# Performance work log

Hardware: AMD Instinct MI355X
Metric: run time of the kernel (lower is better)

Reference implementation:

```python
import jax, jax.numpy as jnp
import numpy as np

NUM_SAMPLE = 10


def setup_inputs() -> dict:
    key = jax.random.key(0)
    k1, k2, k3, k4, k5 = jax.random.split(key, 5)
    N, F, B, S = 100000, 256, 20000, NUM_SAMPLE
    features_ue = jax.random.normal(k1, (N, F), dtype=jnp.float32)
    features_ap = jax.random.normal(k2, (N, F), dtype=jnp.float32)
    neigh_idx = jax.random.randint(k3, (B, S), 0, N, dtype=jnp.int32)
    nodes = jax.random.randint(k4, (B,), 0, N, dtype=jnp.int32)
    # xavier-uniform weight [embed_dim, feature_dim] = [256, 2*F]
    embed_dim, feature_dim = 256, 2 * F
    limit = float(np.sqrt(6.0 / (embed_dim + feature_dim)))
    weight = jax.random.uniform(k5, (embed_dim, feature_dim), dtype=jnp.float32,
                                minval=-limit, maxval=limit)
    return {"features_ue": features_ue, "features_ap": features_ap,
            "neigh_idx": neigh_idx, "nodes": nodes, "weight": weight}


def reference(features_ue, features_ap, neigh_idx, nodes, weight):
    # sample_model='ue2ue': other_feature = self_feature = features_ue
    S = neigh_idx.shape[1]
    # gather sampled neighbor features: [B, S, F] -> sum over S
    gathered = jnp.take(features_ue, neigh_idx, axis=0)
    # original: mask.div(num_neigh + 1), i.e. divide by count PLUS one
    neigh_feats = gathered.sum(axis=1) / jnp.float32(S + 1)  # [B, F]
    self_feats = jnp.take(features_ue, nodes, axis=0)        # [B, F]
    combined = jnp.concatenate([self_feats, neigh_feats], axis=1)  # [B, 2F]
    # weight.mm(combined.t()) then relu -> [embed_dim, B]
    out = jax.nn.relu(jnp.einsum('ef,bf->eb', weight, combined))
    return out
```

## Files before the change

kernel.cpp:

```cpp
#include <hip/hip_runtime.h>

typedef __attribute__((ext_vector_type(8))) short short8;
typedef __attribute__((ext_vector_type(4))) float f32x4;

#define B_TOTAL 20000
#define B_PAD   20096
#define NF      256
#define K2      512
#define NS      10

__device__ __forceinline__ unsigned short f2bf(float x) {
    unsigned u = __builtin_bit_cast(unsigned, x);
    u += 0x7FFFu + ((u >> 16) & 1u);
    return (unsigned short)(u >> 16);
}

__global__ __launch_bounds__(256) void gather_combine(
    const float* __restrict__ ue, const int* __restrict__ nidx,
    const int* __restrict__ nodes, const float* __restrict__ w,
    unsigned short* __restrict__ comb, unsigned short* __restrict__ wbf)
{
    const int t = threadIdx.x, blk = blockIdx.x;
    if (blk < 128) {
        const int base = blk * 1024 + t * 4;
        const float4 v = *(const float4*)(w + base);
        ushort4 o;
        o.x = f2bf(v.x); o.y = f2bf(v.y); o.z = f2bf(v.z); o.w = f2bf(v.w);
        *(ushort4*)(wbf + base) = o;
    }
    const int lane = t & 63;
    const int b = blk * 4 + (t >> 6);
    if (b >= B_PAD) return;
    unsigned short* crow = comb + (size_t)b * K2;
    if (b < B_TOTAL) {
        const int node = nodes[b];
        const float4 sf = ((const float4*)(ue + (size_t)node * NF))[lane];
        int myidx = 0;
        if (lane < NS) myidx = nidx[b * NS + lane];
        float ax = 0.f, ay = 0.f, az = 0.f, aw = 0.f;
        #pragma unroll
        for (int s = 0; s < NS; ++s) {
            const int is = __shfl(myidx, s);
            const float4 v = ((const float4*)(ue + (size_t)is * NF))[lane];
            ax += v.x; ay += v.y; az += v.z; aw += v.w;
        }
        const float inv = 1.0f / 11.0f;
        ushort4 s4, n4;
        s4.x = f2bf(sf.x); s4.y = f2bf(sf.y); s4.z = f2bf(sf.z); s4.w = f2bf(sf.w);
        n4.x = f2bf(ax * inv); n4.y = f2bf(ay * inv); n4.z = f2bf(az * inv); n4.w = f2bf(aw * inv);
        *(ushort4*)(crow + lane * 4) = s4;
        *(ushort4*)(crow + NF + lane * 4) = n4;
    } else {
        ushort4 z; z.x = z.y = z.z = z.w = 0;
        *(ushort4*)(crow + lane * 4) = z;
        *(ushort4*)(crow + NF + lane * 4) = z;
    }
}

__global__ __launch_bounds__(256) void gemm_relu(
    const unsigned short* __restrict__ wbf,
    const unsigned short* __restrict__ comb,
    float* __restrict__ out)
{
    __shared__ unsigned short Alds[4096];
    __shared__ unsigned short Blds[4096];
    const int t    = threadIdx.x;
    const int lane = t & 63;
    const int wv   = t >> 6;
    const int wm   = wv >> 1, wn = wv & 1;
    const int n0   = blockIdx.x * 128;
    const int m0   = blockIdx.y * 128;
    const int srow = t & 127;
    const int skg  = t >> 7;
    const int fr   = lane & 15;
    const int kq   = lane >> 4;

    f32x4 acc[4][4] = {};

    const short8* A8 = (const short8*)Alds;
    const short8* B8 = (const short8*)Blds;

    for (int ks = 0; ks < 16; ++ks) {
        const unsigned short* ga = wbf  + (size_t)(m0 + srow) * K2 + ks * 32 + skg * 8;
        const unsigned short* gb = comb + (size_t)(n0 + srow) * K2 + ks * 32 + skg * 8;
        unsigned short* la = Alds + t * 8;
        unsigned short* lb = Blds + t * 8;
        __builtin_amdgcn_global_load_lds((const __attribute__((address_space(1))) void*)ga,
            (__attribute__((address_space(3))) void*)la, 16, 0, 0);
        __builtin_amdgcn_global_load_lds((const __attribute__((address_space(1))) void*)(ga + 16),
            (__attribute__((address_space(3))) void*)(la + 2048), 16, 0, 0);
        __builtin_amdgcn_global_load_lds((const __attribute__((address_space(1))) void*)gb,
            (__attribute__((address_space(3))) void*)lb, 16, 0, 0);
        __builtin_amdgcn_global_load_lds((const __attribute__((address_space(1))) void*)(gb + 16),
            (__attribute__((address_space(3))) void*)(lb + 2048), 16, 0, 0);
        asm volatile("s_waitcnt vmcnt(0)" ::: "memory");
        __syncthreads();

        short8 af[4], bg[4];
        #pragma unroll
        for (int i = 0; i < 4; ++i)
            af[i] = A8[kq * 128 + wm * 64 + i * 16 + fr];
        #pragma unroll
        for (int j = 0; j < 4; ++j)
            bg[j] = B8[kq * 128 + wn * 64 + j * 16 + fr];
        #pragma unroll
        for (int i = 0; i < 4; ++i)
            #pragma unroll
            for (int j = 0; j < 4; ++j)
                acc[i][j] = __builtin_amdgcn_mfma_f32_16x16x32_bf16(af[i], bg[j], acc[i][j], 0, 0, 0);
        __syncthreads();
    }

    #pragma unroll
    for (int i = 0; i < 4; ++i) {
        const int e = m0 + wm * 64 + i * 16 + kq * 4;
        #pragma unroll
        for (int j = 0; j < 4; ++j) {
            const int b = n0 + wn * 64 + j * 16 + fr;
            if (b < B_TOTAL) {
                #pragma unroll
                for (int r = 0; r < 4; ++r)
                    out[(size_t)(e + r) * B_TOTAL + b] = fmaxf(acc[i][j][r], 0.0f);
            }
        }
    }
}

extern "C" void kernel_launch(void* const* d_in, const int* in_sizes, int n_in,
                              void* d_out, int out_size, void* d_ws, size_t ws_size,
                              hipStream_t stream) {
    const float* ue    = (const float*)d_in[0];
    const int*   nidx  = (const int*)d_in[2];
    const int*   nodes = (const int*)d_in[3];
    const float* w     = (const float*)d_in[4];
    float*       out   = (float*)d_out;

    unsigned short* comb = (unsigned short*)d_ws;
    unsigned short* wbf  = comb + (size_t)B_PAD * K2;

    hipLaunchKernelGGL(gather_combine, dim3(B_PAD / 4), dim3(256), 0, stream,
                       ue, nidx, nodes, w, comb, wbf);
    hipLaunchKernelGGL(gemm_relu, dim3(B_PAD / 128, 2), dim3(256), 0, stream,
                       wbf, comb, out);
}
```

Baseline: 60.64 us.

## Fuse neighbor gather with GEMM, keeping combined tile in swizzled LDS

Weight conversion moves into its own small kernel. The gather/mean and the GEMM are fused: each block gathers 32 batch rows into a swizzled bf16 LDS tile and multiplies it against all 256 weight rows, which are loaded straight from global/L2 into registers. This removes the global round trip of the combined bf16 matrix and the per-k-step syncs. In exchange, each block rereads the whole weight matrix and the tiles are smaller, so the MFMA work per load drops.

```diff
diff --git a/kernel.cpp b/kernel.cpp
--- a/kernel.cpp
+++ b/kernel.cpp
@@ -4,7 +4,8 @@
 typedef __attribute__((ext_vector_type(4))) float f32x4;
 
 #define B_TOTAL 20000
-#define B_PAD   20096
+#define BT      32
+#define NBLK    625
 #define NF      256
 #define K2      512
 #define NS      10
@@ -15,113 +16,97 @@
     return (unsigned short)(u >> 16);
 }
 
-__global__ __launch_bounds__(256) void gather_combine(
-    const float* __restrict__ ue, const int* __restrict__ nidx,
-    const int* __restrict__ nodes, const float* __restrict__ w,
-    unsigned short* __restrict__ comb, unsigned short* __restrict__ wbf)
-{
-    const int t = threadIdx.x, blk = blockIdx.x;
-    if (blk < 128) {
-        const int base = blk * 1024 + t * 4;
-        const float4 v = *(const float4*)(w + base);
-        ushort4 o;
-        o.x = f2bf(v.x); o.y = f2bf(v.y); o.z = f2bf(v.z); o.w = f2bf(v.w);
-        *(ushort4*)(wbf + base) = o;
-    }
-    const int lane = t & 63;
-    const int b = blk * 4 + (t >> 6);
-    if (b >= B_PAD) return;
-    unsigned short* crow = comb + (size_t)b * K2;
-    if (b < B_TOTAL) {
-        const int node = nodes[b];
-        const float4 sf = ((const float4*)(ue + (size_t)node * NF))[lane];
-        int myidx = 0;
-        if (lane < NS) myidx = nidx[b * NS + lane];
-        float ax = 0.f, ay = 0.f, az = 0.f, aw = 0.f;
-        #pragma unroll
-        for (int s = 0; s < NS; ++s) {
-            const int is = __shfl(myidx, s);
-            const float4 v = ((const float4*)(ue + (size_t)is * NF))[lane];
-            ax += v.x; ay += v.y; az += v.z; aw += v.w;
-        }
-        const float inv = 1.0f / 11.0f;
-        ushort4 s4, n4;
-        s4.x = f2bf(sf.x); s4.y = f2bf(sf.y); s4.z = f2bf(sf.z); s4.w = f2bf(sf.w);
-        n4.x = f2bf(ax * inv); n4.y = f2bf(ay * inv); n4.z = f2bf(az * inv); n4.w = f2bf(aw * inv);
-        *(ushort4*)(crow + lane * 4) = s4;
-        *(ushort4*)(crow + NF + lane * 4) = n4;
-    } else {
-        ushort4 z; z.x = z.y = z.z = z.w = 0;
-        *(ushort4*)(crow + lane * 4) = z;
-        *(ushort4*)(crow + NF + lane * 4) = z;
-    }
+__global__ __launch_bounds__(256) void wconvert(const float* __restrict__ w,
+                                                unsigned short* __restrict__ wbf) {
+    const int i = (blockIdx.x * 256 + threadIdx.x) * 4;
+    const float4 v = *(const float4*)(w + i);
+    ushort4 o;
+    o.x = f2bf(v.x); o.y = f2bf(v.y); o.z = f2bf(v.z); o.w = f2bf(v.w);
+    *(ushort4*)(wbf + i) = o;
 }
 
-__global__ __launch_bounds__(256) void gemm_relu(
-    const unsigned short* __restrict__ wbf,
-    const unsigned short* __restrict__ comb,
+__global__ __launch_bounds__(256) void fused(
+    const float* __restrict__ ue, const int* __restrict__ nidx,
+    const int* __restrict__ nodes, const unsigned short* __restrict__ wbf,
     float* __restrict__ out)
 {
-    __shared__ unsigned short Alds[4096];
-    __shared__ unsigned short Blds[4096];
+    __shared__ unsigned short comb[64 * BT * 8];
     const int t    = threadIdx.x;
     const int lane = t & 63;
     const int wv   = t >> 6;
-    const int wm   = wv >> 1, wn = wv & 1;
-    const int n0   = blockIdx.x * 128;
-    const int m0   = blockIdx.y * 128;
-    const int srow = t & 127;
-    const int skg  = t >> 7;
-    const int fr   = lane & 15;
-    const int kq   = lane >> 4;
+    const int n0   = blockIdx.x * BT;
 
-    f32x4 acc[4][4] = {};
+    {
+        const int r0 = wv * 8;
+        const int b0 = n0 + r0;
+        const int idxA = nidx[b0 * NS + lane];
+        const int idxB = (lane < 16) ? nidx[b0 * NS + 64 + lane] : 0;
+        const int nodv = (lane < 8) ? nodes[b0 + lane] : 0;
 
-    const short8* A8 = (const short8*)Alds;
-    const short8* B8 = (const short8*)Blds;
+        const int kcS   = lane >> 1;
+        const int swz   = (kcS & 7) << 4;
+        const int half8 = (lane & 1) * 8;
 
+        #pragma unroll
+        for (int r = 0; r < 8; ++r) {
+            const int row = r0 + r;
+            const int nd  = __shfl(nodv, r);
+            const float4 sf = ((const float4*)(ue + (size_t)nd * NF))[lane];
+            float ax = 0.f, ay = 0.f, az = 0.f, aw = 0.f;
+            #pragma unroll
+            for (int s = 0; s < NS; ++s) {
+                const int p  = r * NS + s;
+                const int is = (p < 64) ? __shfl(idxA, p) : __shfl(idxB, p - 64);
+                const float4 v = ((const float4*)(ue + (size_t)is * NF))[lane];
+                ax += v.x; ay += v.y; az += v.z; aw += v.w;
+            }
+            const float inv = 1.0f / 11.0f;
+            ushort4 s4, n4;
+            s4.x = f2bf(sf.x); s4.y = f2bf(sf.y); s4.z = f2bf(sf.z); s4.w = f2bf(sf.w);
+            n4.x = f2bf(ax * inv); n4.y = f2bf(ay * inv);
+            n4.z = f2bf(az * inv); n4.w = f2bf(aw * inv);
+            const int byteS = (((kcS       ) * BT + row) * 16 + half8) ^ swz;
+            const int byteN = (((kcS + 32  ) * BT + row) * 16 + half8) ^ swz;
+            *(ushort4*)((char*)comb + byteS) = s4;
+            *(ushort4*)((char*)comb + byteN) = n4;
+        }
+    }
+    __syncthreads();
+
+    const int fr = lane & 15;
+    const int kq = lane >> 4;
+    const unsigned short* wp = wbf + (size_t)(wv * 64 + fr) * K2 + kq * 8;
+
+    f32x4 acc[4][2] = {};
+    #pragma unroll
     for (int ks = 0; ks < 16; ++ks) {
-        const unsigned short* ga = wbf  + (size_t)(m0 + srow) * K2 + ks * 32 + skg * 8;
-        const unsigned short* gb = comb + (size_t)(n0 + srow) * K2 + ks * 32 + skg * 8;
-        unsigned short* la = Alds + t * 8;
-        unsigned short* lb = Blds + t * 8;
-        __builtin_amdgcn_global_load_lds((const __attribute__((address_space(1))) void*)ga,
-            (__attribute__((address_space(3))) void*)la, 16, 0, 0);
-        __builtin_amdgcn_global_load_lds((const __attribute__((address_space(1))) void*)(ga + 16),
-            (__attribute__((address_space(3))) void*)(la + 2048), 16, 0, 0);
-        __builtin_amdgcn_global_load_lds((const __attribute__((address_space(1))) void*)gb,
-            (__attribute__((address_space(3))) void*)lb, 16, 0, 0);
-        __builtin_amdgcn_global_load_lds((const __attribute__((address_space(1))) void*)(gb + 16),
-            (__attribute__((address_space(3))) void*)(lb + 2048), 16, 0, 0);
-        asm volatile("s_waitcnt vmcnt(0)" ::: "memory");
-        __syncthreads();
-
-        short8 af[4], bg[4];
+        short8 af[4];
         #pragma unroll
         for (int i = 0; i < 4; ++i)
-            af[i] = A8[kq * 128 + wm * 64 + i * 16 + fr];
+            af[i] = *(const short8*)(wp + (size_t)i * 16 * K2 + ks * 32);
+        short8 bg[2];
+        const int kc = ks * 4 + kq;
         #pragma unroll
-        for (int j = 0; j < 4; ++j)
-            bg[j] = B8[kq * 128 + wn * 64 + j * 16 + fr];
+        for (int j = 0; j < 2; ++j) {
+            const int byte = ((kc * BT + j * 16 + fr) * 16) ^ ((kc & 7) << 4);
+            bg[j] = *(const short8*)((const char*)comb + byte);
+        }
         #pragma unroll
         for (int i = 0; i < 4; ++i)
             #pragma unroll
-            for (int j = 0; j < 4; ++j)
+            for (int j = 0; j < 2; ++j)
                 acc[i][j] = __builtin_amdgcn_mfma_f32_16x16x32_bf16(af[i], bg[j], acc[i][j], 0, 0, 0);
-        __syncthreads();
     }
 
     #pragma unroll
     for (int i = 0; i < 4; ++i) {
-        const int e = m0 + wm * 64 + i * 16 + kq * 4;
+        const int e = wv * 64 + i * 16 + kq * 4;
         #pragma unroll
-        for (int j = 0; j < 4; ++j) {
-            const int b = n0 + wn * 64 + j * 16 + fr;
-            if (b < B_TOTAL) {
-                #pragma unroll
-                for (int r = 0; r < 4; ++r)
-                    out[(size_t)(e + r) * B_TOTAL + b] = fmaxf(acc[i][j][r], 0.0f);
-            }
+        for (int j = 0; j < 2; ++j) {
+            const int b = n0 + j * 16 + fr;
+            #pragma unroll
+            for (int r = 0; r < 4; ++r)
+                out[(size_t)(e + r) * B_TOTAL + b] = fmaxf(acc[i][j][r], 0.0f);
         }
     }
 }
@@ -135,11 +120,9 @@
     const float* w     = (const float*)d_in[4];
     float*       out   = (float*)d_out;
 
-    unsigned short* comb = (unsigned short*)d_ws;
-    unsigned short* wbf  = comb + (size_t)B_PAD * K2;
+    unsigned short* wbf = (unsigned short*)d_ws;
 
-    hipLaunchKernelGGL(gather_combine, dim3(B_PAD / 4), dim3(256), 0, stream,
-                       ue, nidx, nodes, w, comb, wbf);
-    hipLaunchKernelGGL(gemm_relu, dim3(B_PAD / 128, 2), dim3(256), 0, stream,
-                       wbf, comb, out);
+    hipLaunchKernelGGL(wconvert, dim3(128), dim3(256), 0, stream, w, wbf);
+    hipLaunchKernelGGL(fused, dim3(NBLK), dim3(256), 0, stream,
+                       ue, nidx, nodes, wbf, out);
 }
```

Result: slower. 62.38 us (+2.9%).

## Drop LDS staging in GEMM, use small register tiles and unpadded batch

Applied to the files above, without the earlier changes.

The GEMM no longer stages A/B tiles in LDS with barriers. Each wave now loads its bf16 fragments straight from global memory into registers for a 32x32 output tile per wave, which lowers per-block reuse but raises the block count and removes syncthreads. The gather kernel now issues all ten neighbor loads up front using scalar index reads instead of shuffles, and sums them in a tree. Batch padding to 20096 is dropped, so the zero-fill of pad rows and the bounds checks in the epilogue go away. The cost is more redundant global and L2 traffic for weights and combined rows.

```diff
diff --git a/kernel.cpp b/kernel.cpp
--- a/kernel.cpp
+++ b/kernel.cpp
@@ -4,7 +4,6 @@
 typedef __attribute__((ext_vector_type(4))) float f32x4;
 
 #define B_TOTAL 20000
-#define B_PAD   20096
 #define NF      256
 #define K2      512
 #define NS      10
@@ -15,7 +14,11 @@
     return (unsigned short)(u >> 16);
 }
 
-__global__ __launch_bounds__(256) void gather_combine(
+__device__ __forceinline__ float4 add4(float4 a, float4 b) {
+    return make_float4(a.x + b.x, a.y + b.y, a.z + b.z, a.w + b.w);
+}
+
+__global__ __launch_bounds__(256) void gather(
     const float* __restrict__ ue, const int* __restrict__ nidx,
     const int* __restrict__ nodes, const float* __restrict__ w,
     unsigned short* __restrict__ comb, unsigned short* __restrict__ wbf)
@@ -29,32 +32,34 @@
         *(ushort4*)(wbf + base) = o;
     }
     const int lane = t & 63;
-    const int b = blk * 4 + (t >> 6);
-    if (b >= B_PAD) return;
+    const int wv = __builtin_amdgcn_readfirstlane(t >> 6);
+    const int b = blk * 4 + wv;
+    if (b >= B_TOTAL) return;
+
+    const int* ip = nidx + (size_t)b * NS;
+    const int node = nodes[b];
+
+    const float4 sf = ((const float4*)(ue + (size_t)node * NF))[lane];
+    float4 a[NS];
+    #pragma unroll
+    for (int s = 0; s < NS; ++s)
+        a[s] = ((const float4*)(ue + (size_t)ip[s] * NF))[lane];
+
+    float4 s01 = add4(a[0], a[1]), s23 = add4(a[2], a[3]);
+    float4 s45 = add4(a[4], a[5]), s67 = add4(a[6], a[7]);
+    float4 s89 = add4(a[8], a[9]);
+    float4 t0 = add4(s01, s23), t1 = add4(s45, s67);
+    float4 sum = add4(add4(t0, t1), s89);
+
+    const float inv = 1.0f / 11.0f;
+    ushort4 s4, n4;
+    s4.x = f2bf(sf.x); s4.y = f2bf(sf.y); s4.z = f2bf(sf.z); s4.w = f2bf(sf.w);
+    n4.x = f2bf(sum.x * inv); n4.y = f2bf(sum.y * inv);
+    n4.z = f2bf(sum.z * inv); n4.w = f2bf(sum.w * inv);
+
     unsigned short* crow = comb + (size_t)b * K2;
-    if (b < B_TOTAL) {
-        const int node = nodes[b];
-        const float4 sf = ((const float4*)(ue + (size_t)node * NF))[lane];
-        int myidx = 0;
-        if (lane < NS) myidx = nidx[b * NS + lane];
-        float ax = 0.f, ay = 0.f, az = 0.f, aw = 0.f;
-        #pragma unroll
-        for (int s = 0; s < NS; ++s) {
-            const int is = __shfl(myidx, s);
-            const float4 v = ((const float4*)(ue + (size_t)is * NF))[lane];
-            ax += v.x; ay += v.y; az += v.z; aw += v.w;
-        }
-        const float inv = 1.0f / 11.0f;
-        ushort4 s4, n4;
-        s4.x = f2bf(sf.x); s4.y = f2bf(sf.y); s4.z = f2bf(sf.z); s4.w = f2bf(sf.w);
-        n4.x = f2bf(ax * inv); n4.y = f2bf(ay * inv); n4.z = f2bf(az * inv); n4.w = f2bf(aw * inv);
-        *(ushort4*)(crow + lane * 4) = s4;
-        *(ushort4*)(crow + NF + lane * 4) = n4;
-    } else {
-        ushort4 z; z.x = z.y = z.z = z.w = 0;
-        *(ushort4*)(crow + lane * 4) = z;
-        *(ushort4*)(crow + NF + lane * 4) = z;
-    }
+    *(ushort4*)(crow + lane * 4) = s4;
+    *(ushort4*)(crow + NF + lane * 4) = n4;
 }
 
 __global__ __launch_bounds__(256) void gemm_relu(
@@ -62,66 +67,41 @@
     const unsigned short* __restrict__ comb,
     float* __restrict__ out)
 {
-    __shared__ unsigned short Alds[4096];
-    __shared__ unsigned short Blds[4096];
-    const int t    = threadIdx.x;
+    const int t = threadIdx.x;
     const int lane = t & 63;
-    const int wv   = t >> 6;
-    const int wm   = wv >> 1, wn = wv & 1;
-    const int n0   = blockIdx.x * 128;
-    const int m0   = blockIdx.y * 128;
-    const int srow = t & 127;
-    const int skg  = t >> 7;
-    const int fr   = lane & 15;
-    const int kq   = lane >> 4;
+    const int wv = t >> 6;
+    const int n0 = blockIdx.x * 32;
+    const int e0 = blockIdx.y * 128 + wv * 32;
+    const int fr = lane & 15;
+    const int kq = lane >> 4;
 
-    f32x4 acc[4][4] = {};
+    const unsigned short* wp = wbf  + (size_t)(e0 + fr) * K2 + kq * 8;
+    const unsigned short* cp = comb + (size_t)(n0 + fr) * K2 + kq * 8;
 
-    const short8* A8 = (const short8*)Alds;
-    const short8* B8 = (const short8*)Blds;
-
+    f32x4 acc[2][2] = {};
+    #pragma unroll 4
     for (int ks = 0; ks < 16; ++ks) {
-        const unsigned short* ga = wbf  + (size_t)(m0 + srow) * K2 + ks * 32 + skg * 8;
-        const unsigned short* gb = comb + (size_t)(n0 + srow) * K2 + ks * 32 + skg * 8;
-        unsigned short* la = Alds + t * 8;
-        unsigned short* lb = Blds + t * 8;
-        __builtin_amdgcn_global_load_lds((const __attribute__((address_space(1))) void*)ga,
-            (__attribute__((address_space(3))) void*)la, 16, 0, 0);
-        __builtin_amdgcn_global_load_lds((const __attribute__((address_space(1))) void*)(ga + 16),
-            (__attribute__((address_space(3))) void*)(la + 2048), 16, 0, 0);
-        __builtin_amdgcn_global_load_lds((const __attribute__((address_space(1))) void*)gb,
-            (__attribute__((address_space(3))) void*)lb, 16, 0, 0);
-        __builtin_amdgcn_global_load_lds((const __attribute__((address_space(1))) void*)(gb + 16),
-            (__attribute__((address_space(3))) void*)(lb + 2048), 16, 0, 0);
-        asm volatile("s_waitcnt vmcnt(0)" ::: "memory");
-        __syncthreads();
-
-        short8 af[4], bg[4];
+        short8 af[2], bg[2];
+        af[0] = *(const short8*)(wp + ks * 32);
+        af[1] = *(const short8*)(wp + (size_t)16 * K2 + ks * 32);
+        bg[0] = *(const short8*)(cp + ks * 32);
+        bg[1] = *(const short8*)(cp + (size_t)16 * K2 + ks * 32);
         #pragma unroll
-        for (int i = 0; i < 4; ++i)
-            af[i] = A8[kq * 128 + wm * 64 + i * 16 + fr];
-        #pragma unroll
-        for (int j = 0; j < 4; ++j)
-            bg[j] = B8[kq * 128 + wn * 64 + j * 16 + fr];
-        #pragma unroll
-        for (int i = 0; i < 4; ++i)
+        for (int i = 0; i < 2; ++i)
             #pragma unroll
-            for (int j = 0; j < 4; ++j)
+            for (int j = 0; j < 2; ++j)
                 acc[i][j] = __builtin_amdgcn_mfma_f32_16x16x32_bf16(af[i], bg[j], acc[i][j], 0, 0, 0);
-        __syncthreads();
     }
 
     #pragma unroll
-    for (int i = 0; i < 4; ++i) {
-        const int e = m0 + wm * 64 + i * 16 + kq * 4;
+    for (int i = 0; i < 2; ++i) {
+        const int e = e0 + i * 16 + kq * 4;
         #pragma unroll
-        for (int j = 0; j < 4; ++j) {
-            const int b = n0 + wn * 64 + j * 16 + fr;
-            if (b < B_TOTAL) {
-                #pragma unroll
-                for (int r = 0; r < 4; ++r)
-                    out[(size_t)(e + r) * B_TOTAL + b] = fmaxf(acc[i][j][r], 0.0f);
-            }
+        for (int j = 0; j < 2; ++j) {
+            const int b = n0 + j * 16 + fr;
+            #pragma unroll
+            for (int r = 0; r < 4; ++r)
+                out[(size_t)(e + r) * B_TOTAL + b] = fmaxf(acc[i][j][r], 0.0f);
         }
     }
 }
@@ -136,10 +116,10 @@
     float*       out   = (float*)d_out;
 
     unsigned short* comb = (unsigned short*)d_ws;
-    unsigned short* wbf  = comb + (size_t)B_PAD * K2;
+    unsigned short* wbf  = comb + (size_t)B_TOTAL * K2;
 
-    hipLaunchKernelGGL(gather_combine, dim3(B_PAD / 4), dim3(256), 0, stream,
+    hipLaunchKernelGGL(gather, dim3(5000), dim3(256), 0, stream,
                        ue, nidx, nodes, w, comb, wbf);
-    hipLaunchKernelGGL(gemm_relu, dim3(B_PAD / 128, 2), dim3(256), 0, stream,
+    hipLaunchKernelGGL(gemm_relu, dim3(625, 2), dim3(256), 0, stream,
                        wbf, comb, out);
 }
```

Result: slower. 79.87 us (+31.7%).

## Shrink GEMM N-tile to 32 and double K-step to raise block count

Applied to the files above, without the earlier changes.

Changes the GEMM tile from 128x128 to 128x32 per block, with each wave computing a 32x32 sub-tile, and processes 64 K-elements per LDS stage so there are 8 iterations instead of 16. This launches four times as many blocks to fill the GPU's compute units better and halves the number of barriers. The cost is more redundant reloading of the weight tile across blocks and less MFMA work per LDS load. A cosmetic line split in the gather kernel is also included.

```diff
diff --git a/kernel.cpp b/kernel.cpp
--- a/kernel.cpp
+++ b/kernel.cpp
@@ -47,7 +47,8 @@
         const float inv = 1.0f / 11.0f;
         ushort4 s4, n4;
         s4.x = f2bf(sf.x); s4.y = f2bf(sf.y); s4.z = f2bf(sf.z); s4.w = f2bf(sf.w);
-        n4.x = f2bf(ax * inv); n4.y = f2bf(ay * inv); n4.z = f2bf(az * inv); n4.w = f2bf(aw * inv);
+        n4.x = f2bf(ax * inv); n4.y = f2bf(ay * inv);
+        n4.z = f2bf(az * inv); n4.w = f2bf(aw * inv);
         *(ushort4*)(crow + lane * 4) = s4;
         *(ushort4*)(crow + NF + lane * 4) = n4;
     } else {
@@ -62,61 +63,64 @@
     const unsigned short* __restrict__ comb,
     float* __restrict__ out)
 {
-    __shared__ unsigned short Alds[4096];
-    __shared__ unsigned short Blds[4096];
+    __shared__ unsigned short Alds[8192];
+    __shared__ unsigned short Blds[2048];
     const int t    = threadIdx.x;
     const int lane = t & 63;
     const int wv   = t >> 6;
-    const int wm   = wv >> 1, wn = wv & 1;
-    const int n0   = blockIdx.x * 128;
+    const int n0   = blockIdx.x * 32;
     const int m0   = blockIdx.y * 128;
-    const int srow = t & 127;
-    const int skg  = t >> 7;
     const int fr   = lane & 15;
     const int kq   = lane >> 4;
 
-    f32x4 acc[4][4] = {};
-
+    f32x4 acc[2][2] = {};
     const short8* A8 = (const short8*)Alds;
     const short8* B8 = (const short8*)Blds;
 
-    for (int ks = 0; ks < 16; ++ks) {
-        const unsigned short* ga = wbf  + (size_t)(m0 + srow) * K2 + ks * 32 + skg * 8;
-        const unsigned short* gb = comb + (size_t)(n0 + srow) * K2 + ks * 32 + skg * 8;
-        unsigned short* la = Alds + t * 8;
-        unsigned short* lb = Blds + t * 8;
-        __builtin_amdgcn_global_load_lds((const __attribute__((address_space(1))) void*)ga,
-            (__attribute__((address_space(3))) void*)la, 16, 0, 0);
-        __builtin_amdgcn_global_load_lds((const __attribute__((address_space(1))) void*)(ga + 16),
-            (__attribute__((address_space(3))) void*)(la + 2048), 16, 0, 0);
-        __builtin_amdgcn_global_load_lds((const __attribute__((address_space(1))) void*)gb,
-            (__attribute__((address_space(3))) void*)lb, 16, 0, 0);
-        __builtin_amdgcn_global_load_lds((const __attribute__((address_space(1))) void*)(gb + 16),
-            (__attribute__((address_space(3))) void*)(lb + 2048), 16, 0, 0);
+    for (int ks = 0; ks < 8; ++ks) {
+        #pragma unroll
+        for (int L = 0; L < 4; ++L) {
+            const int d16 = L * 256 + t;
+            const int g = d16 >> 7, row = d16 & 127;
+            const unsigned short* src = wbf + (size_t)(m0 + row) * K2 + ks * 64 + g * 8;
+            __builtin_amdgcn_global_load_lds(
+                (const __attribute__((address_space(1))) void*)src,
+                (__attribute__((address_space(3))) void*)(Alds + (size_t)d16 * 8), 16, 0, 0);
+        }
+        {
+            const int g = t >> 5, row = t & 31;
+            const unsigned short* src = comb + (size_t)(n0 + row) * K2 + ks * 64 + g * 8;
+            __builtin_amdgcn_global_load_lds(
+                (const __attribute__((address_space(1))) void*)src,
+                (__attribute__((address_space(3))) void*)(Blds + (size_t)t * 8), 16, 0, 0);
+        }
         asm volatile("s_waitcnt vmcnt(0)" ::: "memory");
         __syncthreads();
 
-        short8 af[4], bg[4];
         #pragma unroll
-        for (int i = 0; i < 4; ++i)
-            af[i] = A8[kq * 128 + wm * 64 + i * 16 + fr];
-        #pragma unroll
-        for (int j = 0; j < 4; ++j)
-            bg[j] = B8[kq * 128 + wn * 64 + j * 16 + fr];
-        #pragma unroll
-        for (int i = 0; i < 4; ++i)
+        for (int h = 0; h < 2; ++h) {
+            short8 af[2], bg[2];
             #pragma unroll
-            for (int j = 0; j < 4; ++j)
-                acc[i][j] = __builtin_amdgcn_mfma_f32_16x16x32_bf16(af[i], bg[j], acc[i][j], 0, 0, 0);
+            for (int i = 0; i < 2; ++i)
+                af[i] = A8[(h * 4 + kq) * 128 + wv * 32 + i * 16 + fr];
+            #pragma unroll
+            for (int j = 0; j < 2; ++j)
+                bg[j] = B8[(h * 4 + kq) * 32 + j * 16 + fr];
+            #pragma unroll
+            for (int i = 0; i < 2; ++i)
+                #pragma unroll
+                for (int j = 0; j < 2; ++j)
+                    acc[i][j] = __builtin_amdgcn_mfma_f32_16x16x32_bf16(af[i], bg[j], acc[i][j], 0, 0, 0);
+        }
         __syncthreads();
     }
 
     #pragma unroll
-    for (int i = 0; i < 4; ++i) {
-        const int e = m0 + wm * 64 + i * 16 + kq * 4;
+    for (int i = 0; i < 2; ++i) {
+        const int e = m0 + wv * 32 + i * 16 + kq * 4;
         #pragma unroll
-        for (int j = 0; j < 4; ++j) {
-            const int b = n0 + wn * 64 + j * 16 + fr;
+        for (int j = 0; j < 2; ++j) {
+            const int b = n0 + j * 16 + fr;
             if (b < B_TOTAL) {
                 #pragma unroll
                 for (int r = 0; r < 4; ++r)
@@ -140,6 +144,6 @@
 
     hipLaunchKernelGGL(gather_combine, dim3(B_PAD / 4), dim3(256), 0, stream,
                        ue, nidx, nodes, w, comb, wbf);
-    hipLaunchKernelGGL(gemm_relu, dim3(B_PAD / 128, 2), dim3(256), 0, stream,
+    hipLaunchKernelGGL(gemm_relu, dim3(B_PAD / 32, 2), dim3(256), 0, stream,
                        wbf, comb, out);
 }
```

Result: slower. 68.16 us (+12.4%).
